# Performance work log

Measured on AMD Instinct MI355X. Metric: run time of the kernel, lower is better.

## Reference

```python
import jax, jax.numpy as jnp
import numpy as np

UP_RATIO = 4

def _gen_grid():
    # gen_grid(4): num_x=num_y=2, linspace(-0.2,0.2,2), meshgrid 'ij'
    g = jnp.array([-0.2, 0.2], dtype=jnp.float32)
    x, y = jnp.meshgrid(g, g, indexing='ij')
    return jnp.stack([x, y], axis=-1).reshape(-1, 2)  # [4, 2]

def setup_inputs() -> dict:
    key = jax.random.key(0)
    ks = jax.random.split(key, 12)
    B, C, N = 8, 128, 1024
    Cin = C + 2            # 130, channels after grid concat
    Cq = Cin // 4          # 32
    sc = 0.05
    f32 = jnp.float32
    inputs = jax.random.normal(ks[0], (B, C, N), f32)
    WF = jax.random.normal(ks[1], (Cq, Cin), f32) * sc
    bF = jnp.zeros((Cq,), f32)
    WG = jax.random.normal(ks[2], (Cq, Cin), f32) * sc
    bG = jnp.zeros((Cq,), f32)
    WH = jax.random.normal(ks[3], (Cin, Cin), f32) * sc
    bH = jnp.zeros((Cin,), f32)
    gamma = jnp.float32(0.5)  # torch inits to 0; nonzero so attention path is exercised
    W1 = jax.random.normal(ks[4], (256, Cin), f32) * sc
    b1 = jnp.zeros((256,), f32)
    W2 = jax.random.normal(ks[5], (128, 256), f32) * sc
    b2 = jnp.zeros((128,), f32)
    return dict(inputs=inputs, WF=WF, bF=bF, WG=WG, bG=bG, WH=WH, bH=bH,
                gamma=gamma, W1=W1, b1=b1, W2=W2, b2=b2)

def _conv1x1(W, b, x):
    # Conv1d(kernel_size=1): x [B,C,M] -> [B,O,M]
    return jnp.einsum('oc,bcm->bom', W, x) + b[:, None]

def reference(inputs, WF, bF, WG, bG, WH, bH, gamma, W1, b1, W2, b2):
    B, C, N = inputs.shape
    up = UP_RATIO
    grid = jnp.repeat(_gen_grid(), N, axis=0)          # [up*N, 2], block-repeated per grid row
    net = jnp.transpose(inputs, (0, 2, 1))             # [B, N, C]
    net = jnp.tile(net, (1, up, 1))                    # [B, up*N, C]
    net = jnp.concatenate([net, jnp.broadcast_to(grid, (B, up * N, 2))], axis=2)
    net = jnp.transpose(net, (0, 2, 1))                # [B, C+2, M]
    # attention_unit
    f = jax.nn.relu(_conv1x1(WF, bF, net))             # [B, 32, M]
    g = jax.nn.relu(_conv1x1(WG, bG, net))             # [B, 32, M]
    h = jax.nn.relu(_conv1x1(WH, bH, net))             # [B, 130, M]
    s = jnp.einsum('bcm,bcn->bmn', g, f)               # g^T f : [B, M, M]
    beta = jax.nn.softmax(s, axis=2)
    o = jnp.einsum('bck,bkm->bcm', h, beta)            # h @ beta
    x = gamma * o + net
    x = jax.nn.relu(_conv1x1(W1, b1, x))               # [B, 256, M]
    x = jax.nn.relu(_conv1x1(W2, b2, x))               # [B, 128, M]
    return x
```

## Files before the change

### kernel.cpp

```cpp
#include <hip/hip_runtime.h>
#include <hip/hip_bf16.h>
#include <math.h>

#define BB    8
#define CC    128
#define NN    1024
#define MM    4096
#define CIN   130
#define CQ    32
#define NROWS 194
#define MPAD  80
#define CIN_P 160


typedef __attribute__((ext_vector_type(8))) short   bf16x8;
typedef __attribute__((ext_vector_type(4))) float   f32x4;
typedef __attribute__((ext_vector_type(8))) unsigned short u16x8;
typedef __attribute__((ext_vector_type(4))) unsigned short u16x4;

static __device__ __forceinline__ unsigned short f2bf(float f) {
    union { float f; unsigned u; } v; v.f = f;
    unsigned r = v.u + 0x7FFFu + ((v.u >> 16) & 1u);
    return (unsigned short)(r >> 16);
}

#define MFMA16(a, b, c) __builtin_amdgcn_mfma_f32_16x16x32_bf16((a), (b), (c), 0, 0, 0)

__global__ __launch_bounds__(256) void prep_kernel(
    const float* __restrict__ W1, const float* __restrict__ W2,
    unsigned short* __restrict__ W1b, unsigned short* __restrict__ W2b)
{
    int i = blockIdx.x * 256 + threadIdx.x;
    if (i < 256 * CIN_P) {
        int o = i / CIN_P, c = i - o * CIN_P;
        W1b[i] = (c < CIN) ? f2bf(W1[o * CIN + c]) : (unsigned short)0;
    } else {
        int j = i - 256 * CIN_P;
        W2b[j] = f2bf(W2[j]);
    }
}

__global__ __launch_bounds__(256) void fgh_kernel(
    const float* __restrict__ inp,
    const float* __restrict__ WF, const float* __restrict__ bF,
    const float* __restrict__ WG, const float* __restrict__ bG,
    const float* __restrict__ WH, const float* __restrict__ bH,
    unsigned short* __restrict__ f_t, unsigned short* __restrict__ g_t,
    unsigned short* __restrict__ h)
{
    const int b  = blockIdx.z;
    const int og = blockIdx.y;
    const int m  = blockIdx.x * 256 + threadIdx.x;

    __shared__ float wl[8][CIN];
    __shared__ float bl[8];

    for (int idx = threadIdx.x; idx < 8 * CIN; idx += 256) {
        int i = idx / CIN, c = idx - i * CIN;
        int o = og * 8 + i;
        float w = 0.f;
        if (o < 32)         w = WF[o * CIN + c];
        else if (o < 64)    w = WG[(o - 32) * CIN + c];
        else if (o < NROWS) w = WH[(o - 64) * CIN + c];
        wl[i][c] = w;
    }
    if (threadIdx.x < 8) {
        int o = og * 8 + threadIdx.x;
        float bv = 0.f;
        if (o < 32)         bv = bF[o];
        else if (o < 64)    bv = bG[o - 32];
        else if (o < NROWS) bv = bH[o - 64];
        bl[threadIdx.x] = bv;
    }
    __syncthreads();

    float acc[8];
    #pragma unroll
    for (int i = 0; i < 8; ++i) acc[i] = bl[i];

    const int mn = m & (NN - 1);
    #pragma unroll 4
    for (int c = 0; c < CC; ++c) {
        float v = inp[((size_t)b * CC + c) * NN + mn];
        #pragma unroll
        for (int i = 0; i < 8; ++i) acc[i] += wl[i][c] * v;
    }
    const int q = m >> 10;
    const float gx = (q >> 1) ? 0.2f : -0.2f;
    const float gy = (q & 1)  ? 0.2f : -0.2f;
    #pragma unroll
    for (int i = 0; i < 8; ++i) acc[i] += wl[i][CC] * gx + wl[i][CC + 1] * gy;

    if (og < 4) {
        u16x8 pk;
        #pragma unroll
        for (int i = 0; i < 8; ++i) pk[i] = f2bf(fmaxf(acc[i], 0.f));
        *(u16x8*)&f_t[((size_t)b * MM + m) * 32 + og * 8] = pk;
    } else if (og < 8) {
        u16x8 pk;
        #pragma unroll
        for (int i = 0; i < 8; ++i) pk[i] = f2bf(fmaxf(acc[i], 0.f));
        *(u16x8*)&g_t[((size_t)b * MM + m) * 32 + (og - 4) * 8] = pk;
    } else {
        #pragma unroll
        for (int i = 0; i < 8; ++i) {
            int o = og * 8 + i;
            if (o < NROWS)
                h[((size_t)b * CIN + (o - 64)) * MM + m] = f2bf(fmaxf(acc[i], 0.f));
        }
    }
}

__global__ __launch_bounds__(256) void rowstats_kernel(
    const unsigned short* __restrict__ f_t, const unsigned short* __restrict__ g_t,
    float* __restrict__ L)
{
    const int b  = blockIdx.y;
    const int k0 = blockIdx.x * 64;
    const int lane = threadIdx.x & 63, w = threadIdx.x >> 6;
    const int l15 = lane & 15, lg = lane >> 4;

    const bf16x8 aG = *(const bf16x8*)&g_t[((size_t)b * MM + k0 + w * 16 + l15) * 32 + lg * 8];
    const f32x4 zero = {0.f, 0.f, 0.f, 0.f};
    f32x4 sum = zero;

    for (int mc = 0; mc < MM; mc += 64) {
        #pragma unroll
        for (int mt = 0; mt < 4; ++mt) {
            bf16x8 fB = *(const bf16x8*)&f_t[((size_t)b * MM + mc + mt * 16 + l15) * 32 + lg * 8];
            f32x4 s = MFMA16(aG, fB, zero);
            #pragma unroll
            for (int r = 0; r < 4; ++r) sum[r] += __expf(s[r] - 4.0f);
        }
    }

    #pragma unroll
    for (int d = 1; d < 16; d <<= 1) {
        #pragma unroll
        for (int r = 0; r < 4; ++r) sum[r] += __shfl_xor(sum[r], d);
    }
    if (l15 == 0) {
        #pragma unroll
        for (int r = 0; r < 4; ++r)
            L[b * MM + k0 + w * 16 + lg * 4 + r] = 4.0f + __logf(sum[r]);
    }
}

__global__ __launch_bounds__(256) void attn_kernel(
    const unsigned short* __restrict__ f_t, const unsigned short* __restrict__ g_t,
    const unsigned short* __restrict__ h,   const float* __restrict__ L,
    const float* __restrict__ inp,          const float* __restrict__ gamma_p,
    unsigned short* __restrict__ x_t)
{
    const int b  = blockIdx.y;
    const int m0 = blockIdx.x * 64;
    const int tid = threadIdx.x;
    const int lane = tid & 63, w = tid >> 6;
    const int l15 = lane & 15, lg = lane >> 4;

    __shared__ unsigned short Hs[144 * MPAD];
    __shared__ unsigned short Et[64 * MPAD];

    const f32x4 zero = {0.f, 0.f, 0.f, 0.f};

    bf16x8 fF[4];
    #pragma unroll
    for (int mt = 0; mt < 4; ++mt)
        fF[mt] = *(const bf16x8*)&f_t[((size_t)b * MM + m0 + mt * 16 + l15) * 32 + lg * 8];

    f32x4 acc[9];
    #pragma unroll
    for (int ct = 0; ct < 9; ++ct) acc[ct] = zero;

    const float gam = gamma_p[0];

    for (int kc = 0; kc < MM; kc += 64) {
        bf16x8 hst[5];
        #pragma unroll
        for (int u = 0; u < 5; ++u) {
            int idx = tid + u * 256;
            int c = idx >> 3, seg = idx & 7;
            bf16x8 v = {0,0,0,0,0,0,0,0};
            if (idx < 1152 && c < CIN)
                v = *(const bf16x8*)&h[((size_t)b * CIN + c) * MM + kc + seg * 8];
            hst[u] = v;
        }

        bf16x8 aG = *(const bf16x8*)&g_t[((size_t)b * MM + kc + w * 16 + l15) * 32 + lg * 8];
        float Lr[4];
        #pragma unroll
        for (int r = 0; r < 4; ++r)
            Lr[r] = L[b * MM + kc + w * 16 + lg * 4 + r];

        f32x4 s[4];
        #pragma unroll
        for (int mt = 0; mt < 4; ++mt)
            s[mt] = MFMA16(aG, fF[mt], zero);

        __syncthreads();

        #pragma unroll
        for (int mt = 0; mt < 4; ++mt) {
            u16x4 pk;
            #pragma unroll
            for (int r = 0; r < 4; ++r) pk[r] = f2bf(__expf(s[mt][r] - Lr[r]));
            *(u16x4*)&Et[(size_t)(mt * 16 + l15) * MPAD + w * 16 + lg * 4] = pk;
        }
        #pragma unroll
        for (int u = 0; u < 5; ++u) {
            int idx = tid + u * 256;
            int c = idx >> 3, seg = idx & 7;
            if (idx < 1152)
                *(bf16x8*)&Hs[(size_t)c * MPAD + seg * 8] = hst[u];
        }
        __syncthreads();

        bf16x8 eB[2];
        #pragma unroll
        for (int ks = 0; ks < 2; ++ks)
            eB[ks] = *(const bf16x8*)&Et[(size_t)(w * 16 + l15) * MPAD + ks * 32 + lg * 8];
        #pragma unroll
        for (int ct = 0; ct < 9; ++ct) {
            #pragma unroll
            for (int ks = 0; ks < 2; ++ks) {
                bf16x8 aH = *(const bf16x8*)&Hs[(size_t)(ct * 16 + l15) * MPAD + ks * 32 + lg * 8];
                acc[ct] = MFMA16(aH, eB[ks], acc[ct]);
            }
        }
    }

    const int m = m0 + w * 16 + l15;
    const int mn = m & (NN - 1);
    const int q = m >> 10;
    const float gx = (q >> 1) ? 0.2f : -0.2f;
    const float gy = (q & 1)  ? 0.2f : -0.2f;

    #pragma unroll
    for (int ct = 0; ct < 9; ++ct) {
        const int cbase = ct * 16 + lg * 4;
        if (cbase < CC) {
            u16x4 pk;
            #pragma unroll
            for (int r = 0; r < 4; ++r) {
                float net = inp[((size_t)b * CC + cbase + r) * NN + mn];
                pk[r] = f2bf(gam * acc[ct][r] + net);
            }
            *(u16x4*)&x_t[((size_t)b * MM + m) * CIN_P + cbase] = pk;
        } else if (cbase == CC) {
            x_t[((size_t)b * MM + m) * CIN_P + CC]     = f2bf(gam * acc[ct][0] + gx);
            x_t[((size_t)b * MM + m) * CIN_P + CC + 1] = f2bf(gam * acc[ct][1] + gy);
        }
    }
}

template <int KS, int OT, bool OUTF32>
__global__ __launch_bounds__(256) void conv_mfma_kernel(
    const unsigned short* __restrict__ Wb, const float* __restrict__ bias,
    const unsigned short* __restrict__ in_t,
    unsigned short* __restrict__ out_bf, float* __restrict__ out_f32)
{
    const int CINP = KS * 32;
    const int lane = threadIdx.x & 63, w = threadIdx.x >> 6;
    const int l15 = lane & 15, lg = lane >> 4;
    const int m = blockIdx.x * 64 + w * 16 + l15;

    bf16x8 bF[KS];
    #pragma unroll
    for (int ks = 0; ks < KS; ++ks)
        bF[ks] = *(const bf16x8*)&in_t[(size_t)m * CINP + ks * 32 + lg * 8];

    const f32x4 zero = {0.f, 0.f, 0.f, 0.f};

    #pragma unroll
    for (int ot = 0; ot < OT; ++ot) {
        f32x4 acc = zero;
        #pragma unroll
        for (int ks = 0; ks < KS; ++ks) {
            bf16x8 aW = *(const bf16x8*)&Wb[(size_t)(ot * 16 + l15) * CINP + ks * 32 + lg * 8];
            acc = MFMA16(aW, bF[ks], acc);
        }
        const int obase = ot * 16 + lg * 4;
        if (OUTF32) {
            const int bb = m >> 12, mm = m & (MM - 1);
            #pragma unroll
            for (int r = 0; r < 4; ++r)
                out_f32[((size_t)bb * (OT * 16) + obase + r) * MM + mm] =
                    fmaxf(acc[r] + bias[obase + r], 0.f);
        } else {
            u16x4 pk;
            #pragma unroll
            for (int r = 0; r < 4; ++r)
                pk[r] = f2bf(fmaxf(acc[r] + bias[obase + r], 0.f));
            *(u16x4*)&out_bf[(size_t)m * (OT * 16) + obase] = pk;
        }
    }
}

extern "C" void kernel_launch(void* const* d_in, const int* in_sizes, int n_in,
                              void* d_out, int out_size, void* d_ws, size_t ws_size,
                              hipStream_t stream)
{
    const float* inp   = (const float*)d_in[0];
    const float* WF    = (const float*)d_in[1];
    const float* bF    = (const float*)d_in[2];
    const float* WG    = (const float*)d_in[3];
    const float* bG    = (const float*)d_in[4];
    const float* WH    = (const float*)d_in[5];
    const float* bH    = (const float*)d_in[6];
    const float* gamma = (const float*)d_in[7];
    const float* W1    = (const float*)d_in[8];
    const float* b1    = (const float*)d_in[9];
    const float* W2    = (const float*)d_in[10];
    const float* b2    = (const float*)d_in[11];
    float* out = (float*)d_out;

    char* p = (char*)d_ws;
    auto alloc = [&](size_t bytes) { char* q = p; p += (bytes + 255) & ~(size_t)255; return q; };
    unsigned short* f_t  = (unsigned short*)alloc((size_t)BB * MM * 32 * 2);
    unsigned short* g_t  = (unsigned short*)alloc((size_t)BB * MM * 32 * 2);
    unsigned short* h    = (unsigned short*)alloc((size_t)BB * CIN * MM * 2);
    float*          L    = (float*)alloc((size_t)BB * MM * 4);
    unsigned short* x_t  = (unsigned short*)alloc((size_t)BB * MM * CIN_P * 2);
    unsigned short* x1_t = (unsigned short*)alloc((size_t)BB * MM * 256 * 2);
    unsigned short* W1b  = (unsigned short*)alloc((size_t)256 * CIN_P * 2);
    unsigned short* W2b  = (unsigned short*)alloc((size_t)128 * 256 * 2);

    prep_kernel<<<288, 256, 0, stream>>>(W1, W2, W1b, W2b);

    fgh_kernel<<<dim3(MM / 256, 25, BB), 256, 0, stream>>>(
        inp, WF, bF, WG, bG, WH, bH, f_t, g_t, h);

    rowstats_kernel<<<dim3(MM / 64, BB), 256, 0, stream>>>(f_t, g_t, L);

    attn_kernel<<<dim3(MM / 64, BB), 256, 0, stream>>>(
        f_t, g_t, h, L, inp, gamma, x_t);

    conv_mfma_kernel<5, 16, false><<<dim3(BB * MM / 64), 256, 0, stream>>>(
        W1b, b1, x_t, x1_t, nullptr);

    conv_mfma_kernel<8, 8, true><<<dim3(BB * MM / 64), 256, 0, stream>>>(
        W2b, b2, x1_t, nullptr, out);
}
```

Before: 307.0 us.

## Split attention and row-stats over key chunks, move f/g/h projection to MFMA

```diff
diff --git a/kernel.cpp b/kernel.cpp
--- a/kernel.cpp
+++ b/kernel.cpp
@@ -7,10 +7,10 @@
 #define NN    1024
 #define MM    4096
 #define CIN   130
-#define CQ    32
 #define NROWS 194
-#define MPAD  80
+#define MPAD  72
 #define CIN_P 160
+#define OPAD  208
 
 
 typedef __attribute__((ext_vector_type(8))) short   bf16x8;
@@ -23,100 +23,146 @@
     unsigned r = v.u + 0x7FFFu + ((v.u >> 16) & 1u);
     return (unsigned short)(r >> 16);
 }
+static __device__ __forceinline__ float bf2f(unsigned short s) {
+    union { unsigned u; float f; } v; v.u = ((unsigned)s) << 16;
+    return v.f;
+}
 
 #define MFMA16(a, b, c) __builtin_amdgcn_mfma_f32_16x16x32_bf16((a), (b), (c), 0, 0, 0)
 
 __global__ __launch_bounds__(256) void prep_kernel(
     const float* __restrict__ W1, const float* __restrict__ W2,
-    unsigned short* __restrict__ W1b, unsigned short* __restrict__ W2b)
+    const float* __restrict__ WF, const float* __restrict__ WG,
+    const float* __restrict__ WH, const float* __restrict__ bFp,
+    const float* __restrict__ bGp, const float* __restrict__ bHp,
+    unsigned short* __restrict__ W1b, unsigned short* __restrict__ W2b,
+    unsigned short* __restrict__ Wfgh, float* __restrict__ bfgh,
+    float* __restrict__ Lsum)
 {
     int i = blockIdx.x * 256 + threadIdx.x;
-    if (i < 256 * CIN_P) {
+    if (i < 40960) {
         int o = i / CIN_P, c = i - o * CIN_P;
         W1b[i] = (c < CIN) ? f2bf(W1[o * CIN + c]) : (unsigned short)0;
-    } else {
-        int j = i - 256 * CIN_P;
+    } else if (i < 73728) {
+        int j = i - 40960;
         W2b[j] = f2bf(W2[j]);
-    }
-}
-
-__global__ __launch_bounds__(256) void fgh_kernel(
-    const float* __restrict__ inp,
-    const float* __restrict__ WF, const float* __restrict__ bF,
-    const float* __restrict__ WG, const float* __restrict__ bG,
-    const float* __restrict__ WH, const float* __restrict__ bH,
+    } else if (i < 107008) {
+        int j = i - 73728;
+        int o = j / CIN_P, c = j - o * CIN_P;
+        float w = 0.f;
+        if (c < CIN) {
+            if (o < 32)         w = WF[o * CIN + c];
+            else if (o < 64)    w = WG[(o - 32) * CIN + c];
+            else if (o < NROWS) w = WH[(o - 64) * CIN + c];
+        }
+        Wfgh[j] = f2bf(w);
+    } else if (i < 107216) {
+        int o = i - 107008;
+        float bv = 0.f;
+        if (o < 32)         bv = bFp[o];
+        else if (o < 64)    bv = bGp[o - 32];
+        else if (o < NROWS) bv = bHp[o - 64];
+        bfgh[o] = bv;
+    } else if (i < 139984) {
+        Lsum[i - 107216] = 0.f;
+    }
+}
+
+__global__ __launch_bounds__(256) void transpose_kernel(
+    const float* __restrict__ inp, unsigned short* __restrict__ net_t)
+{
+    const int b  = blockIdx.y;
+    const int n0 = blockIdx.x * 32;
+    const int t  = threadIdx.x;
+
+    __shared__ float tile[CC][33];
+
+    for (int idx = t; idx < CC * 32; idx += 256) {
+        int c = idx >> 5, n = idx & 31;
+        tile[c][n] = inp[((size_t)b * CC + c) * NN + n0 + n];
+    }
+    __syncthreads();
+
+    const int n = t >> 3, grp = t & 7;
+    #pragma unroll
+    for (int q = 0; q < 4; ++q) {
+        const int m = q * NN + n0 + n;
+        const float gx = (q >> 1) ? 0.2f : -0.2f;
+        const float gy = (q & 1)  ? 0.2f : -0.2f;
+        for (int j = grp; j < 20; j += 8) {
+            const int c0 = j * 8;
+            u16x8 pk;
+            #pragma unroll
+            for (int i = 0; i < 8; ++i) {
+                int c = c0 + i;
+                float v = (c < CC) ? tile[c][n]
+                        : (c == CC) ? gx : (c == CC + 1) ? gy : 0.f;
+                pk[i] = f2bf(v);
+            }
+            *(u16x8*)&net_t[((size_t)b * MM + m) * CIN_P + c0] = pk;
+        }
+    }
+}
+
+__global__ __launch_bounds__(256) void proj_kernel(
+    const unsigned short* __restrict__ Wfgh, const float* __restrict__ bfgh,
+    const unsigned short* __restrict__ net_t,
     unsigned short* __restrict__ f_t, unsigned short* __restrict__ g_t,
     unsigned short* __restrict__ h)
 {
-    const int b  = blockIdx.z;
-    const int og = blockIdx.y;
-    const int m  = blockIdx.x * 256 + threadIdx.x;
-
-    __shared__ float wl[8][CIN];
-    __shared__ float bl[8];
-
-    for (int idx = threadIdx.x; idx < 8 * CIN; idx += 256) {
-        int i = idx / CIN, c = idx - i * CIN;
-        int o = og * 8 + i;
-        float w = 0.f;
-        if (o < 32)         w = WF[o * CIN + c];
-        else if (o < 64)    w = WG[(o - 32) * CIN + c];
-        else if (o < NROWS) w = WH[(o - 64) * CIN + c];
-        wl[i][c] = w;
-    }
-    if (threadIdx.x < 8) {
-        int o = og * 8 + threadIdx.x;
-        float bv = 0.f;
-        if (o < 32)         bv = bF[o];
-        else if (o < 64)    bv = bG[o - 32];
-        else if (o < NROWS) bv = bH[o - 64];
-        bl[threadIdx.x] = bv;
-    }
-    __syncthreads();
-
-    float acc[8];
-    #pragma unroll
-    for (int i = 0; i < 8; ++i) acc[i] = bl[i];
-
-    const int mn = m & (NN - 1);
-    #pragma unroll 4
-    for (int c = 0; c < CC; ++c) {
-        float v = inp[((size_t)b * CC + c) * NN + mn];
-        #pragma unroll
-        for (int i = 0; i < 8; ++i) acc[i] += wl[i][c] * v;
-    }
-    const int q = m >> 10;
-    const float gx = (q >> 1) ? 0.2f : -0.2f;
-    const float gy = (q & 1)  ? 0.2f : -0.2f;
-    #pragma unroll
-    for (int i = 0; i < 8; ++i) acc[i] += wl[i][CC] * gx + wl[i][CC + 1] * gy;
-
-    if (og < 4) {
-        u16x8 pk;
-        #pragma unroll
-        for (int i = 0; i < 8; ++i) pk[i] = f2bf(fmaxf(acc[i], 0.f));
-        *(u16x8*)&f_t[((size_t)b * MM + m) * 32 + og * 8] = pk;
-    } else if (og < 8) {
-        u16x8 pk;
-        #pragma unroll
-        for (int i = 0; i < 8; ++i) pk[i] = f2bf(fmaxf(acc[i], 0.f));
-        *(u16x8*)&g_t[((size_t)b * MM + m) * 32 + (og - 4) * 8] = pk;
-    } else {
-        #pragma unroll
-        for (int i = 0; i < 8; ++i) {
-            int o = og * 8 + i;
-            if (o < NROWS)
-                h[((size_t)b * CIN + (o - 64)) * MM + m] = f2bf(fmaxf(acc[i], 0.f));
+    const int lane = threadIdx.x & 63, w = threadIdx.x >> 6;
+    const int l15 = lane & 15, lg = lane >> 4;
+    const int mg = blockIdx.x * 64 + w * 16 + l15;
+    const int b = mg >> 12, m = mg & (MM - 1);
+
+    bf16x8 nf[5];
+    #pragma unroll
+    for (int ks = 0; ks < 5; ++ks)
+        nf[ks] = *(const bf16x8*)&net_t[(size_t)mg * CIN_P + ks * 32 + lg * 8];
+
+    const f32x4 zero = {0.f, 0.f, 0.f, 0.f};
+
+    #pragma unroll
+    for (int ot = 0; ot < 13; ++ot) {
+        f32x4 acc = zero;
+        #pragma unroll
+        for (int ks = 0; ks < 5; ++ks) {
+            bf16x8 aW = *(const bf16x8*)&Wfgh[(size_t)(ot * 16 + l15) * CIN_P + ks * 32 + lg * 8];
+            acc = MFMA16(aW, nf[ks], acc);
+        }
+        const int o0 = ot * 16 + lg * 4;
+        float v[4];
+        #pragma unroll
+        for (int r = 0; r < 4; ++r) v[r] = fmaxf(acc[r] + bfgh[o0 + r], 0.f);
+
+        if (ot < 2) {
+            u16x4 pk;
+            #pragma unroll
+            for (int r = 0; r < 4; ++r) pk[r] = f2bf(v[r]);
+            *(u16x4*)&f_t[(size_t)mg * 32 + o0] = pk;
+        } else if (ot < 4) {
+            u16x4 pk;
+            #pragma unroll
+            for (int r = 0; r < 4; ++r) pk[r] = f2bf(v[r]);
+            *(u16x4*)&g_t[(size_t)mg * 32 + (o0 - 32)] = pk;
+        } else {
+            #pragma unroll
+            for (int r = 0; r < 4; ++r) {
+                int o = o0 + r;
+                if (o < NROWS)
+                    h[((size_t)b * CIN + (o - 64)) * MM + m] = f2bf(v[r]);
+            }
         }
     }
 }
 
 __global__ __launch_bounds__(256) void rowstats_kernel(
     const unsigned short* __restrict__ f_t, const unsigned short* __restrict__ g_t,
-    float* __restrict__ L)
+    float* __restrict__ Lsum)
 {
     const int b  = blockIdx.y;
     const int k0 = blockIdx.x * 64;
+    const int m0 = blockIdx.z * 1024;
     const int lane = threadIdx.x & 63, w = threadIdx.x >> 6;
     const int l15 = lane & 15, lg = lane >> 4;
 
@@ -124,7 +170,7 @@
     const f32x4 zero = {0.f, 0.f, 0.f, 0.f};
     f32x4 sum = zero;
 
-    for (int mc = 0; mc < MM; mc += 64) {
+    for (int mc = m0; mc < m0 + 1024; mc += 64) {
         #pragma unroll
         for (int mt = 0; mt < 4; ++mt) {
             bf16x8 fB = *(const bf16x8*)&f_t[((size_t)b * MM + mc + mt * 16 + l15) * 32 + lg * 8];
@@ -142,18 +188,18 @@
     if (l15 == 0) {
         #pragma unroll
         for (int r = 0; r < 4; ++r)
-            L[b * MM + k0 + w * 16 + lg * 4 + r] = 4.0f + __logf(sum[r]);
+            atomicAdd(&Lsum[b * MM + k0 + w * 16 + lg * 4 + r], sum[r]);
     }
 }
 
 __global__ __launch_bounds__(256) void attn_kernel(
     const unsigned short* __restrict__ f_t, const unsigned short* __restrict__ g_t,
-    const unsigned short* __restrict__ h,   const float* __restrict__ L,
-    const float* __restrict__ inp,          const float* __restrict__ gamma_p,
-    unsigned short* __restrict__ x_t)
+    const unsigned short* __restrict__ h,   const float* __restrict__ Lsum,
+    float* __restrict__ P)
 {
     const int b  = blockIdx.y;
     const int m0 = blockIdx.x * 64;
+    const int kz = blockIdx.z;
     const int tid = threadIdx.x;
     const int lane = tid & 63, w = tid >> 6;
     const int l15 = lane & 15, lg = lane >> 4;
@@ -172,9 +218,8 @@
     #pragma unroll
     for (int ct = 0; ct < 9; ++ct) acc[ct] = zero;
 
-    const float gam = gamma_p[0];
-
-    for (int kc = 0; kc < MM; kc += 64) {
+    const int kbeg = kz * (MM / 2), kend = kbeg + (MM / 2);
+    for (int kc = kbeg; kc < kend; kc += 64) {
         bf16x8 hst[5];
         #pragma unroll
         for (int u = 0; u < 5; ++u) {
@@ -187,10 +232,10 @@
         }
 
         bf16x8 aG = *(const bf16x8*)&g_t[((size_t)b * MM + kc + w * 16 + l15) * 32 + lg * 8];
-        float Lr[4];
+        float rinv[4];
         #pragma unroll
         for (int r = 0; r < 4; ++r)
-            Lr[r] = L[b * MM + kc + w * 16 + lg * 4 + r];
+            rinv[r] = 1.0f / Lsum[b * MM + kc + w * 16 + lg * 4 + r];
 
         f32x4 s[4];
         #pragma unroll
@@ -203,7 +248,8 @@
         for (int mt = 0; mt < 4; ++mt) {
             u16x4 pk;
             #pragma unroll
-            for (int r = 0; r < 4; ++r) pk[r] = f2bf(__expf(s[mt][r] - Lr[r]));
+            for (int r = 0; r < 4; ++r)
+                pk[r] = f2bf(__expf(s[mt][r] - 4.0f) * rinv[r]);
             *(u16x4*)&Et[(size_t)(mt * 16 + l15) * MPAD + w * 16 + lg * 4] = pk;
         }
         #pragma unroll
@@ -230,26 +276,43 @@
     }
 
     const int m = m0 + w * 16 + l15;
-    const int mn = m & (NN - 1);
-    const int q = m >> 10;
-    const float gx = (q >> 1) ? 0.2f : -0.2f;
-    const float gy = (q & 1)  ? 0.2f : -0.2f;
-
     #pragma unroll
     for (int ct = 0; ct < 9; ++ct) {
-        const int cbase = ct * 16 + lg * 4;
-        if (cbase < CC) {
-            u16x4 pk;
-            #pragma unroll
-            for (int r = 0; r < 4; ++r) {
-                float net = inp[((size_t)b * CC + cbase + r) * NN + mn];
-                pk[r] = f2bf(gam * acc[ct][r] + net);
+        #pragma unroll
+        for (int r = 0; r < 4; ++r) {
+            const int c = ct * 16 + lg * 4 + r;
+            if (c < CIN)
+                P[((size_t)(kz * BB + b) * CIN + c) * MM + m] = acc[ct][r];
+        }
+    }
+}
+
+__global__ __launch_bounds__(256) void combine_kernel(
+    const float* __restrict__ P, const unsigned short* __restrict__ net_t,
+    const float* __restrict__ gamma_p, unsigned short* __restrict__ x_t)
+{
+    const int b = blockIdx.y;
+    const int moff = threadIdx.x & 63, cg = threadIdx.x >> 6;
+    const int m = blockIdx.x * 64 + moff;
+    const float gam = gamma_p[0];
+
+    #pragma unroll
+    for (int j = 0; j < 5; ++j) {
+        const int c0 = cg * 40 + j * 8;
+        u16x8 net8 = *(const u16x8*)&net_t[((size_t)b * MM + m) * CIN_P + c0];
+        u16x8 pk;
+        #pragma unroll
+        for (int i = 0; i < 8; ++i) {
+            const int c = c0 + i;
+            if (c < CIN) {
+                float p0 = P[((size_t)(0 * BB + b) * CIN + c) * MM + m];
+                float p1 = P[((size_t)(1 * BB + b) * CIN + c) * MM + m];
+                pk[i] = f2bf(gam * (p0 + p1) + bf2f(net8[i]));
+            } else {
+                pk[i] = 0;
             }
-            *(u16x4*)&x_t[((size_t)b * MM + m) * CIN_P + cbase] = pk;
-        } else if (cbase == CC) {
-            x_t[((size_t)b * MM + m) * CIN_P + CC]     = f2bf(gam * acc[ct][0] + gx);
-            x_t[((size_t)b * MM + m) * CIN_P + CC + 1] = f2bf(gam * acc[ct][1] + gy);
-        }
+        }
+        *(u16x8*)&x_t[((size_t)b * MM + m) * CIN_P + c0] = pk;
     }
 }
 
@@ -264,10 +327,10 @@
     const int l15 = lane & 15, lg = lane >> 4;
     const int m = blockIdx.x * 64 + w * 16 + l15;
 
-    bf16x8 bF[KS];
+    bf16x8 bFr[KS];
     #pragma unroll
     for (int ks = 0; ks < KS; ++ks)
-        bF[ks] = *(const bf16x8*)&in_t[(size_t)m * CINP + ks * 32 + lg * 8];
+        bFr[ks] = *(const bf16x8*)&in_t[(size_t)m * CINP + ks * 32 + lg * 8];
 
     const f32x4 zero = {0.f, 0.f, 0.f, 0.f};
 
@@ -277,7 +340,7 @@
         #pragma unroll
         for (int ks = 0; ks < KS; ++ks) {
             bf16x8 aW = *(const bf16x8*)&Wb[(size_t)(ot * 16 + l15) * CINP + ks * 32 + lg * 8];
-            acc = MFMA16(aW, bF[ks], acc);
+            acc = MFMA16(aW, bFr[ks], acc);
         }
         const int obase = ot * 16 + lg * 4;
         if (OUTF32) {
@@ -316,24 +379,32 @@
 
     char* p = (char*)d_ws;
     auto alloc = [&](size_t bytes) { char* q = p; p += (bytes + 255) & ~(size_t)255; return q; };
-    unsigned short* f_t  = (unsigned short*)alloc((size_t)BB * MM * 32 * 2);
-    unsigned short* g_t  = (unsigned short*)alloc((size_t)BB * MM * 32 * 2);
-    unsigned short* h    = (unsigned short*)alloc((size_t)BB * CIN * MM * 2);
-    float*          L    = (float*)alloc((size_t)BB * MM * 4);
-    unsigned short* x_t  = (unsigned short*)alloc((size_t)BB * MM * CIN_P * 2);
-    unsigned short* x1_t = (unsigned short*)alloc((size_t)BB * MM * 256 * 2);
-    unsigned short* W1b  = (unsigned short*)alloc((size_t)256 * CIN_P * 2);
-    unsigned short* W2b  = (unsigned short*)alloc((size_t)128 * 256 * 2);
-
-    prep_kernel<<<288, 256, 0, stream>>>(W1, W2, W1b, W2b);
-
-    fgh_kernel<<<dim3(MM / 256, 25, BB), 256, 0, stream>>>(
-        inp, WF, bF, WG, bG, WH, bH, f_t, g_t, h);
-
-    rowstats_kernel<<<dim3(MM / 64, BB), 256, 0, stream>>>(f_t, g_t, L);
-
-    attn_kernel<<<dim3(MM / 64, BB), 256, 0, stream>>>(
-        f_t, g_t, h, L, inp, gamma, x_t);
+    unsigned short* net_t = (unsigned short*)alloc((size_t)BB * MM * CIN_P * 2);
+    unsigned short* f_t   = (unsigned short*)alloc((size_t)BB * MM * 32 * 2);
+    unsigned short* g_t   = (unsigned short*)alloc((size_t)BB * MM * 32 * 2);
+    unsigned short* h     = (unsigned short*)alloc((size_t)BB * CIN * MM * 2);
+    float*          Lsum  = (float*)alloc((size_t)BB * MM * 4);
+    unsigned short* x_t   = (unsigned short*)alloc((size_t)BB * MM * CIN_P * 2);
+    float*          P     = (float*)alloc((size_t)2 * BB * CIN * MM * 4);
+    unsigned short* x1_t  = (unsigned short*)P;
+    unsigned short* W1b   = (unsigned short*)alloc((size_t)256 * CIN_P * 2);
+    unsigned short* W2b   = (unsigned short*)alloc((size_t)128 * 256 * 2);
+    unsigned short* Wfgh  = (unsigned short*)alloc((size_t)OPAD * CIN_P * 2);
+    float*          bfgh  = (float*)alloc((size_t)OPAD * 4);
+
+    prep_kernel<<<547, 256, 0, stream>>>(W1, W2, WF, WG, WH, bF, bG, bH,
+                                         W1b, W2b, Wfgh, bfgh, Lsum);
+
+    transpose_kernel<<<dim3(NN / 32, BB), 256, 0, stream>>>(inp, net_t);
+
+    proj_kernel<<<dim3(BB * MM / 64), 256, 0, stream>>>(
+        Wfgh, bfgh, net_t, f_t, g_t, h);
+
+    rowstats_kernel<<<dim3(MM / 64, BB, 4), 256, 0, stream>>>(f_t, g_t, Lsum);
+
+    attn_kernel<<<dim3(MM / 64, BB, 2), 256, 0, stream>>>(f_t, g_t, h, Lsum, P);
+
+    combine_kernel<<<dim3(MM / 64, BB), 256, 0, stream>>>(P, net_t, gamma, x_t);
 
     conv_mfma_kernel<5, 16, false><<<dim3(BB * MM / 64), 256, 0, stream>>>(
         W1b, b1, x_t, x1_t, nullptr);
```

Result: faster. 298.3 us (-2.8%).
